# Kernel tuning notes

Hardware: AMD Instinct MI355X
Metric: run time of the kernel (lower is better)

## Reference

```python
import jax, jax.numpy as jnp
import numpy as np

B = 64          # graphs per batch
NPG = 4000      # nodes per graph
CPG0 = 400      # level-0 clusters per graph
CPG1 = 40       # level-1 clusters per graph
DEG = 8         # avg degree
F_IN = 64       # node feature dim (input_shape)


def setup_inputs() -> dict:
    rng = np.random.RandomState(0)
    N0 = B * NPG
    E0 = N0 * DEG
    N1 = B * CPG0
    N2 = B * CPG1
    # node -> graph and node -> level-0 cluster (globally consecutive ids)
    node_graph = np.repeat(np.arange(N0 // NPG), NPG)
    local = np.tile(np.arange(NPG), B)
    cluster0 = node_graph * CPG0 + local // (NPG // CPG0)
    # random edges, endpoints within the same graph
    edge_graph = np.repeat(np.arange(B), NPG * DEG)
    src = edge_graph * NPG + rng.randint(0, NPG, size=E0)
    dst = edge_graph * NPG + rng.randint(0, NPG, size=E0)
    edge_index = np.stack([src, dst]).astype(np.int64)
    # community_pooling's pool_edge: map edges through cluster0, drop self-loops,
    # coalesce duplicates (edge_attr summed). Precompute the integer structure.
    ci, cj = cluster0[src], cluster0[dst]
    mask = ci != cj
    key_ = ci.astype(np.int64) * N1 + cj.astype(np.int64)
    uniq, inv = np.unique(key_[mask], return_inverse=True)
    E1 = uniq.shape[0]
    edge_seg = np.full(E0, E1, dtype=np.int64)   # dropped self-loops -> dummy seg E1
    edge_seg[mask] = inv
    edge_index1 = np.stack([uniq // N1, uniq % N1]).astype(np.int64)
    # level-1 clusters on pooled nodes and graph id of each level-1 cluster
    cl_idx = np.arange(N1)
    cluster1 = (cl_idx // CPG0) * CPG1 + (cl_idx % CPG0) // (CPG0 // CPG1)
    batch2 = np.arange(N2) // CPG1

    key = jax.random.key(0)
    ks = jax.random.split(key, 10)

    def lin(k, fin, fout):
        return jax.random.normal(k, (fin, fout), jnp.float32) / np.sqrt(fin)

    return dict(
        x=jax.random.normal(ks[0], (N0, F_IN), jnp.float32),
        edge_attr=jax.random.uniform(ks[1], (E0, 1), jnp.float32),
        edge_index=jnp.asarray(edge_index),
        cluster0=jnp.asarray(cluster0.astype(np.int64)),
        edge_index1=jnp.asarray(edge_index1),
        edge_seg=jnp.asarray(edge_seg),
        cluster1=jnp.asarray(cluster1.astype(np.int64)),
        batch2=jnp.asarray(batch2.astype(np.int64)),
        n_clusters0=N1, n_clusters1=N2, n_graphs=B,
        W1=lin(ks[2], F_IN, 16), We1=lin(ks[3], 1, 1), Wa1=lin(ks[4], 2 * 16 + 1, 1),
        W2=lin(ks[5], 16, 32), We2=lin(ks[6], 1, 1), Wa2=lin(ks[7], 2 * 32 + 1, 1),
        fc1_W=lin(ks[8], 32, 64), fc1_b=jnp.zeros((64,), jnp.float32),
        fc2_W=lin(ks[9], 64, 1), fc2_b=jnp.zeros((1,), jnp.float32),
    )


def _gin_conv(x, edge_index, edge_attr, W, We, Wa, num_nodes):
    # DeepRank-GNN GINetConvLayer (all linears bias-free)
    row, col = edge_index[0], edge_index[1]
    xp = x @ W                      # project once, then gather (same math as fc(x[col]))
    xrow, xcol = xp[row], xp[col]   # (E, out)
    ed = edge_attr @ We             # (E, n_edge_feat)
    alpha = jnp.concatenate([xrow, xcol, ed], axis=1) @ Wa   # (E, 1)
    alpha = jax.nn.leaky_relu(alpha)
    # faithful: softmax over dim=1 of an (E,1) tensor -> all ones
    alpha = jax.nn.softmax(alpha, axis=1)
    h = alpha * xcol
    return jax.ops.segment_sum(h, row, num_segments=num_nodes)


def reference(x, edge_attr, edge_index, cluster0, edge_index1, edge_seg,
              cluster1, batch2, n_clusters0, n_clusters1, n_graphs,
              W1, We1, Wa1, W2, We2, Wa2, fc1_W, fc1_b, fc2_W, fc2_b):
    # conv1 + relu
    x1 = jax.nn.relu(_gin_conv(x, edge_index, edge_attr, W1, We1, Wa1, x.shape[0]))
    # community_pooling: scatter_max nodes onto clusters, coalesced pooled edges
    x_pool = jax.ops.segment_max(x1, cluster0, num_segments=n_clusters0)
    E1 = edge_index1.shape[1]
    ea1 = jax.ops.segment_sum(edge_attr, edge_seg, num_segments=E1 + 1)[:E1]
    # conv2 + relu on pooled graph
    x2 = jax.nn.relu(_gin_conv(x_pool, edge_index1, ea1, W2, We2, Wa2, n_clusters0))
    # max_pool_x over level-1 clusters, then scatter_mean per graph
    x3 = jax.ops.segment_max(x2, cluster1, num_segments=n_clusters1)
    s = jax.ops.segment_sum(x3, batch2, num_segments=n_graphs)
    cnt = jax.ops.segment_sum(jnp.ones((x3.shape[0], 1), x3.dtype), batch2,
                              num_segments=n_graphs)
    xg = s / cnt                                  # (B, 32)
    h = jax.nn.relu(xg @ fc1_W + fc1_b)           # (B, 64)
    return h @ fc2_W + fc2_b                      # (B, 1)
```

## Files before the change

### kernel.cpp

```cpp
#include <hip/hip_runtime.h>


#define C1 16
#define C2 32
#define NPG 4000
#define EPG 32000
#define NPQ 1000
#define ELLW 32
#define SCW 34

__global__ __launch_bounds__(256) void pre_k(const float* __restrict__ x,
                                             const float* __restrict__ W,
                                             float* __restrict__ xp1,
                                             const int* __restrict__ ei1,
                                             int* __restrict__ rp,
                                             int N0, int E1, int N1, int G1) {
    int bid = blockIdx.x;
    int t = threadIdx.x;
    if (bid < G1) {
        __shared__ float xs[64][65];
        __shared__ float Ws[64][16];
        int n0 = bid * 64;
        const float4* xg = (const float4*)(x + (size_t)n0 * 64);
        for (int i = t; i < 1024; i += 256) {
            float4 v = xg[i];
            int r = i >> 4, c4 = (i & 15) * 4;
            xs[r][c4] = v.x; xs[r][c4 + 1] = v.y;
            xs[r][c4 + 2] = v.z; xs[r][c4 + 3] = v.w;
        }
        {
            float4 wv = ((const float4*)W)[t];
            int r = t >> 2, c4 = (t & 3) * 4;
            Ws[r][c4] = wv.x; Ws[r][c4 + 1] = wv.y;
            Ws[r][c4 + 2] = wv.z; Ws[r][c4 + 3] = wv.w;
        }
        __syncthreads();
        int r = t >> 2, q = t & 3;
        float4 acc = make_float4(0.f, 0.f, 0.f, 0.f);
#pragma unroll
        for (int k = 0; k < 64; ++k) {
            float xv = xs[r][k];
            acc.x += xv * Ws[k][q * 4 + 0];
            acc.y += xv * Ws[k][q * 4 + 1];
            acc.z += xv * Ws[k][q * 4 + 2];
            acc.w += xv * Ws[k][q * 4 + 3];
        }
        ((float4*)xp1)[(size_t)(n0 + r) * 4 + q] = acc;
    } else {
        int e = (bid - G1) * 256 + t;
        if (e >= E1) return;
        int r = ei1[e];
        int rprev = __shfl_up(r, 1);
        if ((t & 63) == 0) rprev = (e == 0) ? -1 : ei1[e - 1];
        for (int rr = rprev + 1; rr <= r; ++rr) rp[rr] = e;
        if (e == E1 - 1)
            for (int rr = r + 1; rr <= N1; ++rr) rp[rr] = E1;
    }
}

__global__ __launch_bounds__(1024) void sortagg_k(const int* __restrict__ ei,
                                                  const float* __restrict__ xp1,
                                                  float* __restrict__ xpool,
                                                  int E0, int B, int cpg) {
    __shared__ int cnt[NPQ];
    __shared__ unsigned short sc16[NPQ * SCW];
    __shared__ float4 sums[250][4];
    int g = blockIdx.x % B;
    int q = blockIdx.x / B;
    int t = threadIdx.x;
    const int4* rows4 = (const int4*)(ei + (size_t)g * EPG);
    const int4* cols4 = (const int4*)(ei + E0 + (size_t)g * EPG);
    int gbase = g * NPG;
    int rbase = gbase + q * NPQ;

    for (int i = t; i < NPQ; i += 1024) cnt[i] = 0;
    __syncthreads();
    for (int i = t; i < EPG / 4; i += 1024) {
        int4 r4 = rows4[i];
        int4 c4 = cols4[i];
        int rl, pos;
        rl = r4.x - rbase;
        if ((unsigned)rl < NPQ) {
            pos = atomicAdd(&cnt[rl], 1);
            if (pos < ELLW) sc16[rl * SCW + pos] = (unsigned short)(c4.x - gbase);
        }
        rl = r4.y - rbase;
        if ((unsigned)rl < NPQ) {
            pos = atomicAdd(&cnt[rl], 1);
            if (pos < ELLW) sc16[rl * SCW + pos] = (unsigned short)(c4.y - gbase);
        }
        rl = r4.z - rbase;
        if ((unsigned)rl < NPQ) {
            pos = atomicAdd(&cnt[rl], 1);
            if (pos < ELLW) sc16[rl * SCW + pos] = (unsigned short)(c4.z - gbase);
        }
        rl = r4.w - rbase;
        if ((unsigned)rl < NPQ) {
            pos = atomicAdd(&cnt[rl], 1);
            if (pos < ELLW) sc16[rl * SCW + pos] = (unsigned short)(c4.w - gbase);
        }
    }
    __syncthreads();
    const float4* xp = (const float4*)xp1 + (size_t)gbase * 4;
    int f4 = t & 3;
    int rl = t >> 2;
    for (int p = 0; p < 4; ++p) {
        if (rl < 250) {
            int r = p * 250 + rl;
            int cn = cnt[r];
            const unsigned short* er = &sc16[r * SCW];
            float4 s = make_float4(0.f, 0.f, 0.f, 0.f);
#pragma unroll
            for (int k = 0; k < 16; ++k) {
                if (k < cn) {
                    float4 v = xp[(size_t)er[k] * 4 + f4];
                    s.x += v.x; s.y += v.y; s.z += v.z; s.w += v.w;
                }
            }
            for (int k = 16; k < cn; ++k) {
                float4 v = xp[(size_t)er[k] * 4 + f4];
                s.x += v.x; s.y += v.y; s.z += v.z; s.w += v.w;
            }
            sums[rl][f4] = s;
        }
        __syncthreads();
        if (t < 100) {
            int cl = t >> 2, ff = t & 3;
            float4 m = sums[cl * 10][ff];
#pragma unroll
            for (int k = 1; k < 10; ++k) {
                float4 v = sums[cl * 10 + k][ff];
                m.x = fmaxf(m.x, v.x); m.y = fmaxf(m.y, v.y);
                m.z = fmaxf(m.z, v.z); m.w = fmaxf(m.w, v.w);
            }
            m.x = fmaxf(m.x, 0.f); m.y = fmaxf(m.y, 0.f);
            m.z = fmaxf(m.z, 0.f); m.w = fmaxf(m.w, 0.f);
            ((float4*)xpool)[(size_t)(g * cpg + q * 100 + p * 25 + cl) * 4 + ff] = m;
        }
        __syncthreads();
    }
}

__global__ __launch_bounds__(256) void agg2_k(const int* __restrict__ ei1,
                                              const int* __restrict__ rp,
                                              const float* __restrict__ xpool,
                                              const float* __restrict__ W2,
                                              float* __restrict__ x2acc,
                                              int E1, int B, int cpg) {
    __shared__ float sums[4][C1];
    int g = blockIdx.x % B;
    int c = blockIdx.x / B;
    int t = threadIdx.x;
    int f4 = t & 3;
    int es = (t >> 2) & 15;
    int w = t >> 6;
    int r = g * cpg + c * 4 + w;
    const int* col = ei1 + E1;
    float4 acc = make_float4(0.f, 0.f, 0.f, 0.f);
    int e0 = rp[r], e1e = rp[r + 1];
#pragma unroll
    for (int k = 0; k < 8; ++k) {
        int e = e0 + es + 16 * k;
        if (e < e1e) {
            float4 v = ((const float4*)(xpool + (size_t)col[e] * C1))[f4];
            acc.x += v.x; acc.y += v.y; acc.z += v.z; acc.w += v.w;
        }
    }
    for (int e = e0 + es + 128; e < e1e; e += 16) {
        float4 v = ((const float4*)(xpool + (size_t)col[e] * C1))[f4];
        acc.x += v.x; acc.y += v.y; acc.z += v.z; acc.w += v.w;
    }
#pragma unroll
    for (int off = 4; off <= 32; off <<= 1) {
        acc.x += __shfl_xor(acc.x, off);
        acc.y += __shfl_xor(acc.y, off);
        acc.z += __shfl_xor(acc.z, off);
        acc.w += __shfl_xor(acc.w, off);
    }
    if (es == 0) {
        sums[w][f4 * 4 + 0] = acc.x;
        sums[w][f4 * 4 + 1] = acc.y;
        sums[w][f4 * 4 + 2] = acc.z;
        sums[w][f4 * 4 + 3] = acc.w;
    }
    __syncthreads();
    if (t < 128) {
        int w2 = t >> 5, j = t & 31;
        const float* s = sums[w2];
        float v = 0.f;
#pragma unroll
        for (int k = 0; k < C1; ++k) v += s[k] * W2[k * C2 + j];
        x2acc[(size_t)(g * cpg + c * 4 + w2) * C2 + j] = v;
    }
}

__global__ __launch_bounds__(256) void final_k(const float* __restrict__ x2acc,
                                               const float* __restrict__ fc1W,
                                               const float* __restrict__ fc1b,
                                               const float* __restrict__ fc2W,
                                               const float* __restrict__ fc2b,
                                               float* __restrict__ out, int cpg) {
    __shared__ float xgs[C2];
    int g = blockIdx.x;
    int t = threadIdx.x;
    if (t < C2) xgs[t] = 0.f;
    __syncthreads();
    for (int i = t; i < 40 * C2; i += 256) {
        int cl = i >> 5, f = i & 31;
        const float* base = x2acc + ((size_t)g * cpg + cl * 10) * C2 + f;
        float m = base[0];
#pragma unroll
        for (int k = 1; k < 10; ++k) m = fmaxf(m, base[k * C2]);
        atomicAdd(&xgs[f], fmaxf(m, 0.f));
    }
    __syncthreads();
    if (t < 64) {
        float h = fc1b[t];
#pragma unroll
        for (int f = 0; f < C2; ++f) h += xgs[f] * (1.f / 40.f) * fc1W[f * 64 + t];
        h = fmaxf(h, 0.f);
        float v = h * fc2W[t];
#pragma unroll
        for (int off = 32; off > 0; off >>= 1) v += __shfl_down(v, off);
        if (t == 0) out[g] = v + fc2b[0];
    }
}

extern "C" void kernel_launch(void* const* d_in, const int* in_sizes, int n_in,
                              void* d_out, int out_size, void* d_ws, size_t ws_size,
                              hipStream_t stream) {
    const float* x    = (const float*)d_in[0];
    const int*   ei   = (const int*)d_in[2];
    const int*   ei1  = (const int*)d_in[4];
    const float* W1   = (const float*)d_in[11];
    const float* W2   = (const float*)d_in[14];
    const float* fc1W = (const float*)d_in[17];
    const float* fc1b = (const float*)d_in[18];
    const float* fc2W = (const float*)d_in[19];
    const float* fc2b = (const float*)d_in[20];
    float* out = (float*)d_out;

    const int N0 = in_sizes[0] / 64;
    const int E0 = in_sizes[2] / 2;
    const int E1 = in_sizes[4] / 2;
    const int N1 = in_sizes[6];
    const int N2 = in_sizes[7];
    const int B  = N2 / 40;
    const int CPG0 = N1 / B;

    float* xp1   = (float*)d_ws;
    float* xpool = xp1 + (size_t)N0 * C1;
    float* x2acc = xpool + (size_t)N1 * C1;
    int*   rp1   = (int*)(x2acc + (size_t)N1 * C2);

    const int G1 = N0 / 64;
    const int RB = (E1 + 255) / 256;

    pre_k<<<G1 + RB, 256, 0, stream>>>(x, W1, xp1, ei1, rp1, N0, E1, N1, G1);
    sortagg_k<<<B * (NPG / NPQ), 1024, 0, stream>>>(ei, xp1, xpool, E0, B, CPG0);
    agg2_k<<<B * (CPG0 / 4), 256, 0, stream>>>(ei1, rp1, xpool, W2, x2acc, E1, B, CPG0);
    final_k<<<B, 256, 0, stream>>>(x2acc, fc1W, fc1b, fc2W, fc2b, out, CPG0);
}
```

Before: 220.1 us.

## Fuse conv2 aggregation with final pooling and MLP; restructure sortagg pooling

Merges the agg2 and final kernels into one per-graph kernel that keeps conv2 outputs in shared memory, so the x2acc buffer no longer makes a global round trip and one launch is removed. The row-pointer build moves from pre_k into extra blocks of sortagg_k. sortagg_k's pooling loop now has 800 threads each take five node rows and combine with a shuffle-max, instead of four phases with block barriers. The fused kernel runs only 64 blocks of 1024 threads, which may leave the GPU underused during the level-1 gather.

```diff
diff --git a/kernel.cpp b/kernel.cpp
--- a/kernel.cpp
+++ b/kernel.cpp
@@ -11,63 +11,62 @@
 
 __global__ __launch_bounds__(256) void pre_k(const float* __restrict__ x,
                                              const float* __restrict__ W,
-                                             float* __restrict__ xp1,
-                                             const int* __restrict__ ei1,
-                                             int* __restrict__ rp,
-                                             int N0, int E1, int N1, int G1) {
+                                             float* __restrict__ xp1) {
+    __shared__ float xs[64][65];
+    __shared__ float Ws[64][16];
+    int t = threadIdx.x;
+    int n0 = blockIdx.x * 64;
+    const float4* xg = (const float4*)(x + (size_t)n0 * 64);
+    for (int i = t; i < 1024; i += 256) {
+        float4 v = xg[i];
+        int r = i >> 4, c4 = (i & 15) * 4;
+        xs[r][c4] = v.x; xs[r][c4 + 1] = v.y;
+        xs[r][c4 + 2] = v.z; xs[r][c4 + 3] = v.w;
+    }
+    {
+        float4 wv = ((const float4*)W)[t];
+        int r = t >> 2, c4 = (t & 3) * 4;
+        Ws[r][c4] = wv.x; Ws[r][c4 + 1] = wv.y;
+        Ws[r][c4 + 2] = wv.z; Ws[r][c4 + 3] = wv.w;
+    }
+    __syncthreads();
+    int r = t >> 2, q = t & 3;
+    float4 acc = make_float4(0.f, 0.f, 0.f, 0.f);
+#pragma unroll
+    for (int k = 0; k < 64; ++k) {
+        float xv = xs[r][k];
+        acc.x += xv * Ws[k][q * 4 + 0];
+        acc.y += xv * Ws[k][q * 4 + 1];
+        acc.z += xv * Ws[k][q * 4 + 2];
+        acc.w += xv * Ws[k][q * 4 + 3];
+    }
+    ((float4*)xp1)[(size_t)(n0 + r) * 4 + q] = acc;
+}
+
+__global__ __launch_bounds__(1024) void sortagg_k(const int* __restrict__ ei,
+                                                  const float* __restrict__ xp1,
+                                                  float* __restrict__ xpool,
+                                                  const int* __restrict__ ei1,
+                                                  int* __restrict__ rp1,
+                                                  int E0, int E1, int N1,
+                                                  int B, int cpg) {
+    __shared__ int cnt[NPQ];
+    __shared__ unsigned short sc16[NPQ * SCW];
     int bid = blockIdx.x;
     int t = threadIdx.x;
-    if (bid < G1) {
-        __shared__ float xs[64][65];
-        __shared__ float Ws[64][16];
-        int n0 = bid * 64;
-        const float4* xg = (const float4*)(x + (size_t)n0 * 64);
-        for (int i = t; i < 1024; i += 256) {
-            float4 v = xg[i];
-            int r = i >> 4, c4 = (i & 15) * 4;
-            xs[r][c4] = v.x; xs[r][c4 + 1] = v.y;
-            xs[r][c4 + 2] = v.z; xs[r][c4 + 3] = v.w;
-        }
-        {
-            float4 wv = ((const float4*)W)[t];
-            int r = t >> 2, c4 = (t & 3) * 4;
-            Ws[r][c4] = wv.x; Ws[r][c4 + 1] = wv.y;
-            Ws[r][c4 + 2] = wv.z; Ws[r][c4 + 3] = wv.w;
-        }
-        __syncthreads();
-        int r = t >> 2, q = t & 3;
-        float4 acc = make_float4(0.f, 0.f, 0.f, 0.f);
-#pragma unroll
-        for (int k = 0; k < 64; ++k) {
-            float xv = xs[r][k];
-            acc.x += xv * Ws[k][q * 4 + 0];
-            acc.y += xv * Ws[k][q * 4 + 1];
-            acc.z += xv * Ws[k][q * 4 + 2];
-            acc.w += xv * Ws[k][q * 4 + 3];
-        }
-        ((float4*)xp1)[(size_t)(n0 + r) * 4 + q] = acc;
-    } else {
-        int e = (bid - G1) * 256 + t;
+    if (bid >= 256) {
+        int e = (bid - 256) * 1024 + t;
         if (e >= E1) return;
         int r = ei1[e];
         int rprev = __shfl_up(r, 1);
         if ((t & 63) == 0) rprev = (e == 0) ? -1 : ei1[e - 1];
-        for (int rr = rprev + 1; rr <= r; ++rr) rp[rr] = e;
+        for (int rr = rprev + 1; rr <= r; ++rr) rp1[rr] = e;
         if (e == E1 - 1)
-            for (int rr = r + 1; rr <= N1; ++rr) rp[rr] = E1;
-    }
-}
-
-__global__ __launch_bounds__(1024) void sortagg_k(const int* __restrict__ ei,
-                                                  const float* __restrict__ xp1,
-                                                  float* __restrict__ xpool,
-                                                  int E0, int B, int cpg) {
-    __shared__ int cnt[NPQ];
-    __shared__ unsigned short sc16[NPQ * SCW];
-    __shared__ float4 sums[250][4];
-    int g = blockIdx.x % B;
-    int q = blockIdx.x / B;
-    int t = threadIdx.x;
+            for (int rr = r + 1; rr <= N1; ++rr) rp1[rr] = E1;
+        return;
+    }
+    int g = bid % B;
+    int q = bid / B;
     const int4* rows4 = (const int4*)(ei + (size_t)g * EPG);
     const int4* cols4 = (const int4*)(ei + E0 + (size_t)g * EPG);
     int gbase = g * NPG;
@@ -101,12 +100,13 @@
         }
     }
     __syncthreads();
-    const float4* xp = (const float4*)xp1 + (size_t)gbase * 4;
-    int f4 = t & 3;
-    int rl = t >> 2;
-    for (int p = 0; p < 4; ++p) {
-        if (rl < 250) {
-            int r = p * 250 + rl;
+    if (t < 800) {
+        int cl = t >> 3, f4 = (t >> 1) & 3, h = t & 1;
+        const float4* xp = (const float4*)xp1 + (size_t)gbase * 4;
+        float4 m = make_float4(-1e30f, -1e30f, -1e30f, -1e30f);
+#pragma unroll
+        for (int j = 0; j < 5; ++j) {
+            int r = cl * 10 + h * 5 + j;
             int cn = cnt[r];
             const unsigned short* er = &sc16[r * SCW];
             float4 s = make_float4(0.f, 0.f, 0.f, 0.f);
@@ -121,96 +121,86 @@
                 float4 v = xp[(size_t)er[k] * 4 + f4];
                 s.x += v.x; s.y += v.y; s.z += v.z; s.w += v.w;
             }
-            sums[rl][f4] = s;
-        }
-        __syncthreads();
-        if (t < 100) {
-            int cl = t >> 2, ff = t & 3;
-            float4 m = sums[cl * 10][ff];
-#pragma unroll
-            for (int k = 1; k < 10; ++k) {
-                float4 v = sums[cl * 10 + k][ff];
-                m.x = fmaxf(m.x, v.x); m.y = fmaxf(m.y, v.y);
-                m.z = fmaxf(m.z, v.z); m.w = fmaxf(m.w, v.w);
-            }
+            m.x = fmaxf(m.x, s.x); m.y = fmaxf(m.y, s.y);
+            m.z = fmaxf(m.z, s.z); m.w = fmaxf(m.w, s.w);
+        }
+        m.x = fmaxf(m.x, __shfl_xor(m.x, 1));
+        m.y = fmaxf(m.y, __shfl_xor(m.y, 1));
+        m.z = fmaxf(m.z, __shfl_xor(m.z, 1));
+        m.w = fmaxf(m.w, __shfl_xor(m.w, 1));
+        if (h == 0) {
             m.x = fmaxf(m.x, 0.f); m.y = fmaxf(m.y, 0.f);
             m.z = fmaxf(m.z, 0.f); m.w = fmaxf(m.w, 0.f);
-            ((float4*)xpool)[(size_t)(g * cpg + q * 100 + p * 25 + cl) * 4 + ff] = m;
-        }
-        __syncthreads();
-    }
-}
-
-__global__ __launch_bounds__(256) void agg2_k(const int* __restrict__ ei1,
-                                              const int* __restrict__ rp,
-                                              const float* __restrict__ xpool,
-                                              const float* __restrict__ W2,
-                                              float* __restrict__ x2acc,
-                                              int E1, int B, int cpg) {
-    __shared__ float sums[4][C1];
-    int g = blockIdx.x % B;
-    int c = blockIdx.x / B;
-    int t = threadIdx.x;
-    int f4 = t & 3;
-    int es = (t >> 2) & 15;
-    int w = t >> 6;
-    int r = g * cpg + c * 4 + w;
-    const int* col = ei1 + E1;
-    float4 acc = make_float4(0.f, 0.f, 0.f, 0.f);
-    int e0 = rp[r], e1e = rp[r + 1];
-#pragma unroll
-    for (int k = 0; k < 8; ++k) {
-        int e = e0 + es + 16 * k;
-        if (e < e1e) {
-            float4 v = ((const float4*)(xpool + (size_t)col[e] * C1))[f4];
-            acc.x += v.x; acc.y += v.y; acc.z += v.z; acc.w += v.w;
-        }
-    }
-    for (int e = e0 + es + 128; e < e1e; e += 16) {
-        float4 v = ((const float4*)(xpool + (size_t)col[e] * C1))[f4];
-        acc.x += v.x; acc.y += v.y; acc.z += v.z; acc.w += v.w;
-    }
-#pragma unroll
-    for (int off = 4; off <= 32; off <<= 1) {
-        acc.x += __shfl_xor(acc.x, off);
-        acc.y += __shfl_xor(acc.y, off);
-        acc.z += __shfl_xor(acc.z, off);
-        acc.w += __shfl_xor(acc.w, off);
-    }
-    if (es == 0) {
-        sums[w][f4 * 4 + 0] = acc.x;
-        sums[w][f4 * 4 + 1] = acc.y;
-        sums[w][f4 * 4 + 2] = acc.z;
-        sums[w][f4 * 4 + 3] = acc.w;
-    }
-    __syncthreads();
-    if (t < 128) {
-        int w2 = t >> 5, j = t & 31;
-        const float* s = sums[w2];
-        float v = 0.f;
-#pragma unroll
-        for (int k = 0; k < C1; ++k) v += s[k] * W2[k * C2 + j];
-        x2acc[(size_t)(g * cpg + c * 4 + w2) * C2 + j] = v;
-    }
-}
-
-__global__ __launch_bounds__(256) void final_k(const float* __restrict__ x2acc,
-                                               const float* __restrict__ fc1W,
-                                               const float* __restrict__ fc1b,
-                                               const float* __restrict__ fc2W,
-                                               const float* __restrict__ fc2b,
-                                               float* __restrict__ out, int cpg) {
+            ((float4*)xpool)[(size_t)(g * cpg + q * 100 + cl) * 4 + f4] = m;
+        }
+    }
+}
+
+__global__ __launch_bounds__(1024) void aggfin_k(const int* __restrict__ ei1,
+                                                 const int* __restrict__ rp,
+                                                 const float* __restrict__ xpool,
+                                                 const float* __restrict__ W2,
+                                                 const float* __restrict__ fc1W,
+                                                 const float* __restrict__ fc1b,
+                                                 const float* __restrict__ fc2W,
+                                                 const float* __restrict__ fc2b,
+                                                 float* __restrict__ out,
+                                                 int E1, int cpg) {
+    __shared__ float sums[400][C1];
+    __shared__ float x2s[400][C2];
+    __shared__ float W2s[C1][C2];
     __shared__ float xgs[C2];
     int g = blockIdx.x;
     int t = threadIdx.x;
+    if (t < 512) ((float*)W2s)[t] = W2[t];
     if (t < C2) xgs[t] = 0.f;
-    __syncthreads();
-    for (int i = t; i < 40 * C2; i += 256) {
+    int lane = t & 63, w = t >> 6;
+    int f4 = lane & 3, es = lane >> 2;
+    const int* col = ei1 + E1;
+    for (int rl = w; rl < 400; rl += 16) {
+        int r = g * cpg + rl;
+        int e0 = rp[r], e1e = rp[r + 1];
+        float4 acc = make_float4(0.f, 0.f, 0.f, 0.f);
+#pragma unroll
+        for (int k = 0; k < 8; ++k) {
+            int e = e0 + es + 16 * k;
+            if (e < e1e) {
+                float4 v = ((const float4*)(xpool + (size_t)col[e] * C1))[f4];
+                acc.x += v.x; acc.y += v.y; acc.z += v.z; acc.w += v.w;
+            }
+        }
+        for (int e = e0 + es + 128; e < e1e; e += 16) {
+            float4 v = ((const float4*)(xpool + (size_t)col[e] * C1))[f4];
+            acc.x += v.x; acc.y += v.y; acc.z += v.z; acc.w += v.w;
+        }
+#pragma unroll
+        for (int off = 4; off <= 32; off <<= 1) {
+            acc.x += __shfl_xor(acc.x, off);
+            acc.y += __shfl_xor(acc.y, off);
+            acc.z += __shfl_xor(acc.z, off);
+            acc.w += __shfl_xor(acc.w, off);
+        }
+        if (es == 0) {
+            sums[rl][f4 * 4 + 0] = acc.x;
+            sums[rl][f4 * 4 + 1] = acc.y;
+            sums[rl][f4 * 4 + 2] = acc.z;
+            sums[rl][f4 * 4 + 3] = acc.w;
+        }
+    }
+    __syncthreads();
+    for (int i = t; i < 400 * C2; i += 1024) {
+        int rl = i >> 5, j = i & 31;
+        float v = 0.f;
+#pragma unroll
+        for (int k = 0; k < C1; ++k) v += sums[rl][k] * W2s[k][j];
+        x2s[rl][j] = v;
+    }
+    __syncthreads();
+    for (int i = t; i < 40 * C2; i += 1024) {
         int cl = i >> 5, f = i & 31;
-        const float* base = x2acc + ((size_t)g * cpg + cl * 10) * C2 + f;
-        float m = base[0];
-#pragma unroll
-        for (int k = 1; k < 10; ++k) m = fmaxf(m, base[k * C2]);
+        float m = x2s[cl * 10][f];
+#pragma unroll
+        for (int k = 1; k < 10; ++k) m = fmaxf(m, x2s[cl * 10 + k][f]);
         atomicAdd(&xgs[f], fmaxf(m, 0.f));
     }
     __syncthreads();
@@ -250,14 +240,13 @@
 
     float* xp1   = (float*)d_ws;
     float* xpool = xp1 + (size_t)N0 * C1;
-    float* x2acc = xpool + (size_t)N1 * C1;
-    int*   rp1   = (int*)(x2acc + (size_t)N1 * C2);
-
-    const int G1 = N0 / 64;
-    const int RB = (E1 + 255) / 256;
-
-    pre_k<<<G1 + RB, 256, 0, stream>>>(x, W1, xp1, ei1, rp1, N0, E1, N1, G1);
-    sortagg_k<<<B * (NPG / NPQ), 1024, 0, stream>>>(ei, xp1, xpool, E0, B, CPG0);
-    agg2_k<<<B * (CPG0 / 4), 256, 0, stream>>>(ei1, rp1, xpool, W2, x2acc, E1, B, CPG0);
-    final_k<<<B, 256, 0, stream>>>(x2acc, fc1W, fc1b, fc2W, fc2b, out, CPG0);
-}
+    int*   rp1   = (int*)(xpool + (size_t)N1 * C1);
+
+    const int RB = (E1 + 1023) / 1024;
+
+    pre_k<<<N0 / 64, 256, 0, stream>>>(x, W1, xp1);
+    sortagg_k<<<256 + RB, 1024, 0, stream>>>(ei, xp1, xpool, ei1, rp1,
+                                             E0, E1, N1, B, CPG0);
+    aggfin_k<<<B, 1024, 0, stream>>>(ei1, rp1, xpool, W2, fc1W, fc1b,
+                                     fc2W, fc2b, out, E1, CPG0);
+}
```

After: 284.0 us. +29.0%, slower.
